# Kernel optimization log

Hardware: AMD Instinct MI355X
Metric: run time of the kernel (lower is better)

## Reference

```python
import jax, jax.numpy as jnp
import numpy as np

B, S = 128, 4096            # batch, num memory slots
W_NUM = 10000               # word_num (vocab)
CONT, FEAT, LSTM = 256, 256, 256
AH, CH = 128, 128           # actor/critic hidden dims
EPS = 1e-8


def _lin(key, out_d, in_d):
    k1, k2 = jax.random.split(key)
    s = 1.0 / np.sqrt(in_d)
    W = jax.random.uniform(k1, (out_d, in_d), jnp.float32, -s, s)
    b = jax.random.uniform(k2, (out_d,), jnp.float32, -s, s)
    return W, b


def setup_inputs() -> dict:
    key = jax.random.key(0)
    ks = jax.random.split(key, 18)
    d = {}
    d['x'] = jax.random.normal(ks[0], (B, W_NUM), jnp.float32)
    d['feat'] = jax.random.normal(ks[1], (B, S, FEAT), jnp.float32)
    d['h_tm1'] = jax.random.normal(ks[2], (B, LSTM), jnp.float32)
    d['c_tm1'] = jax.random.normal(ks[3], (B, LSTM), jnp.float32)
    d['W_x2cont'], d['b_x2cont'] = _lin(ks[4], CONT, W_NUM)
    d['W_h2cont'], d['b_h2cont'] = _lin(ks[5], CONT, LSTM)
    d['W_cont2key'], d['b_cont2key'] = _lin(ks[6], FEAT, CONT)
    d['W_cont2strength'], d['b_cont2strength'] = _lin(ks[7], 1, CONT)
    d['W_att_gates'], d['b_att_gates'] = _lin(ks[8], 1, FEAT + LSTM + CONT)
    d['W_ih'], d['b_ih'] = _lin(ks[9], 4 * LSTM, CONT + FEAT)
    d['W_hh'], d['b_hh'] = _lin(ks[10], 4 * LSTM, LSTM)
    d['W_actor_hid'], d['b_actor_hid'] = _lin(ks[11], AH, LSTM)
    d['W_critic_hid'], d['b_critic_hid'] = _lin(ks[12], CH, LSTM)
    d['W_actor'], d['b_actor'] = _lin(ks[13], W_NUM, AH)
    d['W_critic'], d['b_critic'] = _lin(ks[14], 1, CH)
    return d


def reference(x, feat, h_tm1, c_tm1,
              W_x2cont, b_x2cont, W_h2cont, b_h2cont,
              W_cont2key, b_cont2key, W_cont2strength, b_cont2strength,
              W_att_gates, b_att_gates, W_ih, b_ih, W_hh, b_hh,
              W_actor_hid, b_actor_hid, W_critic_hid, b_critic_hid,
              W_actor, b_actor, W_critic, b_critic):
    lin = lambda v, W, b: v @ W.T + b
    # controller
    x_cont = lin(x, W_x2cont, b_x2cont)                      # [B, CONT]
    h_cont = lin(h_tm1, W_h2cont, b_h2cont)                  # [B, CONT]
    control = jax.nn.relu(x_cont + h_cont)
    key_v = jnp.tanh(lin(control, W_cont2key, b_cont2key))   # [B, FEAT]
    strength = jax.nn.relu(lin(control, W_cont2strength, b_cont2strength)) + 1.0  # [B,1]
    # NTM-style content addressing: sharpened cosine similarity -> softmax over slots
    feat_n = jnp.linalg.norm(feat, axis=-1)                  # [B, S]
    key_n = jnp.linalg.norm(key_v, axis=-1, keepdims=True)   # [B, 1]
    sim = jnp.einsum('bsd,bd->bs', feat, key_v) / (feat_n * key_n + EPS)
    alpha = jax.nn.softmax(strength * sim, axis=-1)          # [B, S]
    cand_att_vec = jnp.einsum('bs,bsd->bd', alpha, feat)     # [B, FEAT]
    # attention gate
    gate_in = jnp.concatenate([cand_att_vec, h_tm1, x_cont], axis=1)  # [B, FEAT+LSTM+CONT]
    gates_att = jax.nn.sigmoid(lin(gate_in, W_att_gates, b_att_gates))
    att_vec = cand_att_vec * gates_att
    # LSTM cell (PyTorch gate order: i, f, g, o)
    inp_lstm = jnp.concatenate([att_vec, x_cont], axis=1)    # [B, FEAT+CONT]
    g = lin(inp_lstm, W_ih, b_ih) + lin(h_tm1, W_hh, b_hh)
    i, f, gg, o = jnp.split(g, 4, axis=1)
    c = jax.nn.sigmoid(f) * c_tm1 + jax.nn.sigmoid(i) * jnp.tanh(gg)
    h = jax.nn.sigmoid(o) * jnp.tanh(c)
    # heads
    action_logit = lin(jax.nn.relu(lin(h, W_actor_hid, b_actor_hid)), W_actor, b_actor)
    value = lin(jax.nn.relu(lin(h, W_critic_hid, b_critic_hid)), W_critic, b_critic)
    return (action_logit, value, h, c)
```

## Files before the change

kernel.cpp:

```cpp
#include <hip/hip_runtime.h>
#include <cmath>


#define B_ 128
#define S_ 4096
#define WN 10000
#define CD 256

__global__ __launch_bounds__(256) void k1_xcont(
    const float* __restrict__ x, const float* __restrict__ Wx,
    float* __restrict__ part) {
  const int nt = blockIdx.x;
  const int ks = blockIdx.y;
  const int t = threadIdx.x;
  __shared__ float xs[128][72];
  __shared__ float wsW[32][72];
  const int o0 = nt * 32;
  const int og = t & 7, bg = t >> 3;
  float acc[4][4] = {{0.f}};
  for (int sub = 0; sub < 4; ++sub) {
    const int k0 = ks * 256 + sub * 64;
    for (int q = t; q < 2048; q += 256) {
      const int row = q >> 4, c4 = q & 15;
      const int k = k0 + c4 * 4;
      float4 v = make_float4(0.f, 0.f, 0.f, 0.f);
      if (k < WN) v = *(const float4*)(x + (size_t)row * WN + k);
      *(float4*)&xs[row][c4 * 4] = v;
    }
    for (int q = t; q < 512; q += 256) {
      const int row = q >> 4, c4 = q & 15;
      const int k = k0 + c4 * 4;
      float4 v = make_float4(0.f, 0.f, 0.f, 0.f);
      if (k < WN) v = *(const float4*)(Wx + (size_t)(o0 + row) * WN + k);
      *(float4*)&wsW[row][c4 * 4] = v;
    }
    __syncthreads();
    for (int k = 0; k < 64; k += 4) {
      float4 wv[4];
#pragma unroll
      for (int i = 0; i < 4; ++i) wv[i] = *(const float4*)&wsW[og * 4 + i][k];
#pragma unroll
      for (int j = 0; j < 4; ++j) {
        float4 xv = *(const float4*)&xs[bg * 4 + j][k];
#pragma unroll
        for (int i = 0; i < 4; ++i)
          acc[j][i] += xv.x * wv[i].x + xv.y * wv[i].y + xv.z * wv[i].z + xv.w * wv[i].w;
      }
    }
    __syncthreads();
  }
#pragma unroll
  for (int j = 0; j < 4; ++j) {
    const int bb = bg * 4 + j;
#pragma unroll
    for (int i = 0; i < 4; ++i)
      part[(size_t)ks * 32768 + bb * 256 + o0 + og * 4 + i] = acc[j][i];
  }
}

__global__ __launch_bounds__(256) void k2_controller(
    const float* __restrict__ part, const float* __restrict__ bx,
    const float* __restrict__ h_tm1, const float* __restrict__ Wh,
    const float* __restrict__ bh, const float* __restrict__ Wk,
    const float* __restrict__ bk, const float* __restrict__ Ws,
    const float* __restrict__ bs, float* __restrict__ x_cont,
    float* __restrict__ key_v, float* __restrict__ strength,
    float* __restrict__ key_n) {
  const int b = blockIdx.x, t = threadIdx.x;
  __shared__ float hs[256], cs[256];
  __shared__ float r1[4], r2[4];
  hs[t] = h_tm1[b * 256 + t];
  float xc = bx[t];
  for (int ks = 0; ks < 40; ++ks) xc += part[(size_t)ks * 32768 + b * 256 + t];
  x_cont[b * 256 + t] = xc;
  __syncthreads();
  float hc = bh[t];
  {
    const float* w = Wh + (size_t)t * 256;
    for (int k = 0; k < 256; k += 4) {
      float4 wv = *(const float4*)(w + k);
      hc += hs[k] * wv.x + hs[k + 1] * wv.y + hs[k + 2] * wv.z + hs[k + 3] * wv.w;
    }
  }
  const float ctl = fmaxf(xc + hc, 0.f);
  cs[t] = ctl;
  __syncthreads();
  float kvv = bk[t];
  {
    const float* w = Wk + (size_t)t * 256;
    for (int k = 0; k < 256; k += 4) {
      float4 wv = *(const float4*)(w + k);
      kvv += cs[k] * wv.x + cs[k + 1] * wv.y + cs[k + 2] * wv.z + cs[k + 3] * wv.w;
    }
  }
  kvv = tanhf(kvv);
  key_v[b * 256 + t] = kvv;
  float v1 = kvv * kvv;
  float v2 = ctl * Ws[t];
  for (int off = 32; off; off >>= 1) {
    v1 += __shfl_xor(v1, off);
    v2 += __shfl_xor(v2, off);
  }
  const int w_ = t >> 6, lane = t & 63;
  if (lane == 0) { r1[w_] = v1; r2[w_] = v2; }
  __syncthreads();
  if (t == 0) {
    const float n2 = r1[0] + r1[1] + r1[2] + r1[3];
    const float sd = r2[0] + r2[1] + r2[2] + r2[3];
    key_n[b] = sqrtf(n2);
    strength[b] = fmaxf(sd + bs[0], 0.f) + 1.f;
  }
}

__global__ __launch_bounds__(256) void k3_attn(
    const float* __restrict__ feat, const float* __restrict__ key_v,
    const float* __restrict__ strength, const float* __restrict__ key_n,
    float* __restrict__ att_part) {
  const int ss = blockIdx.x;
  const int b = blockIdx.y;
  const int t = threadIdx.x;
  const int w = t >> 6, lane = t & 63;
  const float str = strength[b];
  const float kn = key_n[b];
  const float4 kv = *(const float4*)(key_v + b * 256 + lane * 4);
  const float* fb = feat + ((size_t)b * S_ + (size_t)ss * 512) * 256;
  float m = -1e30f, l = 0.f;
  float4 o = make_float4(0.f, 0.f, 0.f, 0.f);
  for (int i = 0; i < 128; ++i) {
    const float4 f = *(const float4*)(fb + (size_t)(i * 4 + w) * 256 + lane * 4);
    float d = f.x * kv.x + f.y * kv.y + f.z * kv.z + f.w * kv.w;
    float n2 = f.x * f.x + f.y * f.y + f.z * f.z + f.w * f.w;
    for (int off = 32; off; off >>= 1) {
      d += __shfl_xor(d, off);
      n2 += __shfl_xor(n2, off);
    }
    const float score = str * d / (sqrtf(n2) * kn + 1e-8f);
    const float mn = fmaxf(m, score);
    const float corr = __expf(m - mn);
    const float alpha = __expf(score - mn);
    l = l * corr + alpha;
    o.x = o.x * corr + alpha * f.x;
    o.y = o.y * corr + alpha * f.y;
    o.z = o.z * corr + alpha * f.z;
    o.w = o.w * corr + alpha * f.w;
    m = mn;
  }
  __shared__ float wm[4], wl[4];
  __shared__ float wo[4][256];
  if (lane == 0) { wm[w] = m; wl[w] = l; }
  *(float4*)&wo[w][lane * 4] = o;
  __syncthreads();
  const float mg = fmaxf(fmaxf(wm[0], wm[1]), fmaxf(wm[2], wm[3]));
  float accd = 0.f;
#pragma unroll
  for (int q = 0; q < 4; ++q) accd += wo[q][t] * __expf(wm[q] - mg);
  float* apo = att_part + (size_t)(b * 8 + ss) * 258;
  if (t == 0) {
    float lt = 0.f;
    for (int q = 0; q < 4; ++q) lt += wl[q] * __expf(wm[q] - mg);
    apo[0] = mg;
    apo[1] = lt;
  }
  apo[2 + t] = accd;
}

__global__ __launch_bounds__(256) void k4a_gate(
    const float* __restrict__ att_part, const float* __restrict__ h_tm1,
    const float* __restrict__ x_cont, const float* __restrict__ Wg,
    const float* __restrict__ bg_, float* __restrict__ inp_cat) {
  const int b = blockIdx.x, t = threadIdx.x;
  const float* ap = att_part + (size_t)b * 8 * 258;
  float mg = -1e30f;
  for (int ss = 0; ss < 8; ++ss) mg = fmaxf(mg, ap[ss * 258]);
  float lg = 0.f, od = 0.f;
  for (int ss = 0; ss < 8; ++ss) {
    const float fct = __expf(ap[ss * 258] - mg);
    lg += ap[ss * 258 + 1] * fct;
    od += ap[ss * 258 + 2 + t] * fct;
  }
  const float cand = od / lg;
  const float hv = h_tm1[b * 256 + t];
  const float xc = x_cont[b * 256 + t];
  float v = cand * Wg[t] + hv * Wg[256 + t] + xc * Wg[512 + t];
  for (int off = 32; off; off >>= 1) v += __shfl_xor(v, off);
  __shared__ float rr[4];
  __shared__ float gsh;
  const int w_ = t >> 6, lane = t & 63;
  if (lane == 0) rr[w_] = v;
  __syncthreads();
  if (t == 0) {
    const float s = rr[0] + rr[1] + rr[2] + rr[3] + bg_[0];
    gsh = 1.f / (1.f + expf(-s));
  }
  __syncthreads();
  inp_cat[b * 768 + t] = cand * gsh;
  inp_cat[b * 768 + 256 + t] = xc;
  inp_cat[b * 768 + 512 + t] = hv;
}

__global__ __launch_bounds__(256) void k4b_lstm(
    const float* __restrict__ inp_cat, const float* __restrict__ Wih,
    const float* __restrict__ bih, const float* __restrict__ Whh,
    const float* __restrict__ bhh, const float* __restrict__ c_tm1,
    float* __restrict__ h_out, float* __restrict__ c_out) {
  const int j0 = blockIdx.x * 2;
  const int t = threadIdx.x;
  __shared__ float inp_s[128][132];
  __shared__ float w_s[8][132];
  const int b = t >> 1, half = t & 1;
  float acc[4] = {0.f, 0.f, 0.f, 0.f};
  for (int kc = 0; kc < 6; ++kc) {
    const int kbase = kc * 128;
    for (int q = t; q < 4096; q += 256) {
      const int row = q >> 5, c4 = q & 31;
      *(float4*)&inp_s[row][c4 * 4] =
          *(const float4*)(inp_cat + (size_t)row * 768 + kbase + c4 * 4);
    }
    {
      const int row = t >> 5, c4 = t & 31;
      const int gate = row & 3;
      const int j = j0 + (row >> 2);
      const int og = gate * 256 + j;
      const int kg = kbase + c4 * 4;
      float4 v;
      if (kg < 512) v = *(const float4*)(Wih + (size_t)og * 512 + kg);
      else          v = *(const float4*)(Whh + (size_t)og * 256 + (kg - 512));
      *(float4*)&w_s[row][c4 * 4] = v;
    }
    __syncthreads();
    for (int k = 0; k < 128; k += 4) {
      const float4 iv = *(const float4*)&inp_s[b][k];
#pragma unroll
      for (int g = 0; g < 4; ++g) {
        const float4 wv = *(const float4*)&w_s[half * 4 + g][k];
        acc[g] += iv.x * wv.x + iv.y * wv.y + iv.z * wv.z + iv.w * wv.w;
      }
    }
    __syncthreads();
  }
  const int j = j0 + half;
  const float gi = acc[0] + bih[j] + bhh[j];
  const float gf = acc[1] + bih[256 + j] + bhh[256 + j];
  const float gg = acc[2] + bih[512 + j] + bhh[512 + j];
  const float go = acc[3] + bih[768 + j] + bhh[768 + j];
  const float ct = c_tm1[b * 256 + j];
  const float i_ = 1.f / (1.f + expf(-gi));
  const float f_ = 1.f / (1.f + expf(-gf));
  const float g_ = tanhf(gg);
  const float o_ = 1.f / (1.f + expf(-go));
  const float c = f_ * ct + i_ * g_;
  const float h = o_ * tanhf(c);
  h_out[b * 256 + j] = h;
  c_out[b * 256 + j] = c;
}

__global__ __launch_bounds__(256) void k5_hid(
    const float* __restrict__ h_in, const float* __restrict__ Wah,
    const float* __restrict__ bah, const float* __restrict__ Wch,
    const float* __restrict__ bch, float* __restrict__ hidA,
    float* __restrict__ hidC) {
  const int b = blockIdx.x, t = threadIdx.x;
  __shared__ float hs[256];
  hs[t] = h_in[b * 256 + t];
  __syncthreads();
  const float* W = (t < 128) ? (Wah + (size_t)t * 256) : (Wch + (size_t)(t - 128) * 256);
  float s = (t < 128) ? bah[t] : bch[t - 128];
  for (int k = 0; k < 256; k += 4) {
    const float4 w = *(const float4*)(W + k);
    s += hs[k] * w.x + hs[k + 1] * w.y + hs[k + 2] * w.z + hs[k + 3] * w.w;
  }
  s = fmaxf(s, 0.f);
  if (t < 128) hidA[b * 128 + t] = s;
  else         hidC[b * 128 + (t - 128)] = s;
}

__global__ __launch_bounds__(256) void k6_heads(
    const float* __restrict__ hidA, const float* __restrict__ hidC,
    const float* __restrict__ Wa, const float* __restrict__ ba,
    const float* __restrict__ Wc, const float* __restrict__ bc,
    float* __restrict__ logits, float* __restrict__ value) {
  const int t = threadIdx.x;
  if (blockIdx.x == 157) {
    if (t < 128) {
      const float* hc = hidC + (size_t)t * 128;
      float s = bc[0];
      for (int k = 0; k < 128; k += 4) {
        const float4 w = *(const float4*)(Wc + k);
        s += hc[k] * w.x + hc[k + 1] * w.y + hc[k + 2] * w.z + hc[k + 3] * w.w;
      }
      value[t] = s;
    }
    return;
  }
  const int o0 = blockIdx.x * 64;
  __shared__ float ha[128][132];
  __shared__ float wa[64][132];
  for (int q = t; q < 4096; q += 256) {
    const int row = q >> 5, c4 = q & 31;
    *(float4*)&ha[row][c4 * 4] = *(const float4*)(hidA + (size_t)row * 128 + c4 * 4);
  }
  for (int q = t; q < 2048; q += 256) {
    const int row = q >> 5, c4 = q & 31;
    const int o = o0 + row;
    float4 v = make_float4(0.f, 0.f, 0.f, 0.f);
    if (o < WN) v = *(const float4*)(Wa + (size_t)o * 128 + c4 * 4);
    *(float4*)&wa[row][c4 * 4] = v;
  }
  __syncthreads();
  const int og = t & 15, bq = t >> 4;
  float acc[8][4];
#pragma unroll
  for (int r = 0; r < 8; ++r)
#pragma unroll
    for (int i = 0; i < 4; ++i) acc[r][i] = 0.f;
  for (int k = 0; k < 128; k += 4) {
    float4 wv[4];
#pragma unroll
    for (int i = 0; i < 4; ++i) wv[i] = *(const float4*)&wa[og * 4 + i][k];
#pragma unroll
    for (int r = 0; r < 8; ++r) {
      const float4 hv = *(const float4*)&ha[bq * 8 + r][k];
#pragma unroll
      for (int i = 0; i < 4; ++i)
        acc[r][i] += hv.x * wv[i].x + hv.y * wv[i].y + hv.z * wv[i].z + hv.w * wv[i].w;
    }
  }
  const int obase = o0 + og * 4;
#pragma unroll
  for (int r = 0; r < 8; ++r) {
    const int bb = bq * 8 + r;
    if (obase + 3 < WN) {
      const float4 bias = *(const float4*)(ba + obase);
      float4 res;
      res.x = acc[r][0] + bias.x;
      res.y = acc[r][1] + bias.y;
      res.z = acc[r][2] + bias.z;
      res.w = acc[r][3] + bias.w;
      *(float4*)(logits + (size_t)bb * WN + obase) = res;
    } else {
      for (int i = 0; i < 4; ++i)
        if (obase + i < WN) logits[(size_t)bb * WN + obase + i] = acc[r][i] + ba[obase + i];
    }
  }
}

extern "C" void kernel_launch(void* const* d_in, const int* in_sizes, int n_in,
                              void* d_out, int out_size, void* d_ws, size_t ws_size,
                              hipStream_t stream) {
  const float* x     = (const float*)d_in[0];
  const float* feat  = (const float*)d_in[1];
  const float* h_tm1 = (const float*)d_in[2];
  const float* c_tm1 = (const float*)d_in[3];
  const float* Wx2c  = (const float*)d_in[4];
  const float* bx2c  = (const float*)d_in[5];
  const float* Wh2c  = (const float*)d_in[6];
  const float* bh2c  = (const float*)d_in[7];
  const float* Wc2k  = (const float*)d_in[8];
  const float* bc2k  = (const float*)d_in[9];
  const float* Wc2s  = (const float*)d_in[10];
  const float* bc2s  = (const float*)d_in[11];
  const float* Wag   = (const float*)d_in[12];
  const float* bag   = (const float*)d_in[13];
  const float* Wih   = (const float*)d_in[14];
  const float* bih   = (const float*)d_in[15];
  const float* Whh   = (const float*)d_in[16];
  const float* bhh   = (const float*)d_in[17];
  const float* Wah   = (const float*)d_in[18];
  const float* bah   = (const float*)d_in[19];
  const float* Wch   = (const float*)d_in[20];
  const float* bch   = (const float*)d_in[21];
  const float* Wa    = (const float*)d_in[22];
  const float* ba    = (const float*)d_in[23];
  const float* Wc    = (const float*)d_in[24];
  const float* bc    = (const float*)d_in[25];

  float* out    = (float*)d_out;
  float* logits = out;
  float* value  = out + 1280000;
  float* h_out  = out + 1280128;
  float* c_out  = out + 1312896;

  float* wsf      = (float*)d_ws;
  float* part     = wsf;
  float* x_cont   = part + 1310720;
  float* key_v    = x_cont + 32768;
  float* strength = key_v + 32768;
  float* key_n    = strength + 128;
  float* att_part = key_n + 128;
  float* inp_cat  = att_part + 264192;
  float* hidA     = inp_cat + 98304;
  float* hidC     = hidA + 16384;

  k1_xcont<<<dim3(8, 40), 256, 0, stream>>>(x, Wx2c, part);
  k2_controller<<<128, 256, 0, stream>>>(part, bx2c, h_tm1, Wh2c, bh2c,
                                         Wc2k, bc2k, Wc2s, bc2s,
                                         x_cont, key_v, strength, key_n);
  k3_attn<<<dim3(8, 128), 256, 0, stream>>>(feat, key_v, strength, key_n, att_part);
  k4a_gate<<<128, 256, 0, stream>>>(att_part, h_tm1, x_cont, Wag, bag, inp_cat);
  k4b_lstm<<<128, 256, 0, stream>>>(inp_cat, Wih, bih, Whh, bhh, c_tm1, h_out, c_out);
  k5_hid<<<128, 256, 0, stream>>>(h_out, Wah, bah, Wch, bch, hidA, hidC);
  k6_heads<<<158, 256, 0, stream>>>(hidA, hidC, Wa, ba, Wc, bc, logits, value);
}
```

Measured before the change: 293.3 us.

## Drop online-softmax max tracking, split attention finer, swizzle LDS in GEMMs

The attention kernel replaces online softmax with a fixed shift by the strength, which bounds the score because cosine similarity is at most one. This removes the running max and correction exponentials, and each block now covers 256 slots with two independent accumulators, launched as 16 splits. The x-projection GEMM is retiled to 16 outputs per block, giving twice as many blocks, and both it and the actor-head GEMM use XOR-swizzled float4 shared memory to avoid bank conflicts. The reduce kernel now just sums the partials. Risks include underflow if strength is large, and extra workspace for the larger partial buffer.

```diff
diff --git a/kernel.cpp b/kernel.cpp
--- a/kernel.cpp
+++ b/kernel.cpp
@@ -13,11 +13,13 @@
   const int nt = blockIdx.x;
   const int ks = blockIdx.y;
   const int t = threadIdx.x;
-  __shared__ float xs[128][72];
-  __shared__ float wsW[32][72];
-  const int o0 = nt * 32;
-  const int og = t & 7, bg = t >> 3;
-  float acc[4][4] = {{0.f}};
+  __shared__ float4 xs[128][16];
+  __shared__ float4 wsW[16][16];
+  const int o0 = nt * 16;
+  const int og = t & 3;
+  const int bg = t >> 2;
+  const int bgx = bg & 7;
+  float acc[2][4] = {{0.f, 0.f, 0.f, 0.f}, {0.f, 0.f, 0.f, 0.f}};
   for (int sub = 0; sub < 4; ++sub) {
     const int k0 = ks * 256 + sub * 64;
     for (int q = t; q < 2048; q += 256) {
@@ -25,23 +27,24 @@
       const int k = k0 + c4 * 4;
       float4 v = make_float4(0.f, 0.f, 0.f, 0.f);
       if (k < WN) v = *(const float4*)(x + (size_t)row * WN + k);
-      *(float4*)&xs[row][c4 * 4] = v;
-    }
-    for (int q = t; q < 512; q += 256) {
-      const int row = q >> 4, c4 = q & 15;
+      xs[row][c4 ^ (row & 7)] = v;
+    }
+    {
+      const int row = t >> 4, c4 = t & 15;
       const int k = k0 + c4 * 4;
       float4 v = make_float4(0.f, 0.f, 0.f, 0.f);
       if (k < WN) v = *(const float4*)(Wx + (size_t)(o0 + row) * WN + k);
-      *(float4*)&wsW[row][c4 * 4] = v;
+      wsW[row][c4 ^ (row & 7)] = v;
     }
     __syncthreads();
-    for (int k = 0; k < 64; k += 4) {
+#pragma unroll
+    for (int c4 = 0; c4 < 16; ++c4) {
       float4 wv[4];
 #pragma unroll
-      for (int i = 0; i < 4; ++i) wv[i] = *(const float4*)&wsW[og * 4 + i][k];
-#pragma unroll
-      for (int j = 0; j < 4; ++j) {
-        float4 xv = *(const float4*)&xs[bg * 4 + j][k];
+      for (int i = 0; i < 4; ++i) wv[i] = wsW[og * 4 + i][c4 ^ ((og * 4 + i) & 7)];
+#pragma unroll
+      for (int j = 0; j < 2; ++j) {
+        const float4 xv = xs[bg + j * 64][c4 ^ bgx];
 #pragma unroll
         for (int i = 0; i < 4; ++i)
           acc[j][i] += xv.x * wv[i].x + xv.y * wv[i].y + xv.z * wv[i].z + xv.w * wv[i].w;
@@ -50,8 +53,8 @@
     __syncthreads();
   }
 #pragma unroll
-  for (int j = 0; j < 4; ++j) {
-    const int bb = bg * 4 + j;
+  for (int j = 0; j < 2; ++j) {
+    const int bb = bg + j * 64;
 #pragma unroll
     for (int i = 0; i < 4; ++i)
       part[(size_t)ks * 32768 + bb * 256 + o0 + og * 4 + i] = acc[j][i];
@@ -112,7 +115,7 @@
   }
 }
 
-__global__ __launch_bounds__(256) void k3_attn(
+__global__ __launch_bounds__(256, 8) void k3_attn(
     const float* __restrict__ feat, const float* __restrict__ key_v,
     const float* __restrict__ strength, const float* __restrict__ key_n,
     float* __restrict__ att_part) {
@@ -123,45 +126,41 @@
   const float str = strength[b];
   const float kn = key_n[b];
   const float4 kv = *(const float4*)(key_v + b * 256 + lane * 4);
-  const float* fb = feat + ((size_t)b * S_ + (size_t)ss * 512) * 256;
-  float m = -1e30f, l = 0.f;
-  float4 o = make_float4(0.f, 0.f, 0.f, 0.f);
-  for (int i = 0; i < 128; ++i) {
-    const float4 f = *(const float4*)(fb + (size_t)(i * 4 + w) * 256 + lane * 4);
-    float d = f.x * kv.x + f.y * kv.y + f.z * kv.z + f.w * kv.w;
-    float n2 = f.x * f.x + f.y * f.y + f.z * f.z + f.w * f.w;
+  const float* fb = feat + ((size_t)b * S_ + (size_t)ss * 256) * 256;
+  float l0 = 0.f, l1 = 0.f;
+  float4 o0 = make_float4(0.f, 0.f, 0.f, 0.f);
+  float4 o1 = make_float4(0.f, 0.f, 0.f, 0.f);
+  for (int i = 0; i < 32; ++i) {
+    const float4 fA = *(const float4*)(fb + (size_t)((i * 2) * 4 + w) * 256 + lane * 4);
+    const float4 fB = *(const float4*)(fb + (size_t)((i * 2 + 1) * 4 + w) * 256 + lane * 4);
+    float dA = fA.x * kv.x + fA.y * kv.y + fA.z * kv.z + fA.w * kv.w;
+    float nA = fA.x * fA.x + fA.y * fA.y + fA.z * fA.z + fA.w * fA.w;
+    float dB = fB.x * kv.x + fB.y * kv.y + fB.z * kv.z + fB.w * kv.w;
+    float nB = fB.x * fB.x + fB.y * fB.y + fB.z * fB.z + fB.w * fB.w;
+#pragma unroll
     for (int off = 32; off; off >>= 1) {
-      d += __shfl_xor(d, off);
-      n2 += __shfl_xor(n2, off);
-    }
-    const float score = str * d / (sqrtf(n2) * kn + 1e-8f);
-    const float mn = fmaxf(m, score);
-    const float corr = __expf(m - mn);
-    const float alpha = __expf(score - mn);
-    l = l * corr + alpha;
-    o.x = o.x * corr + alpha * f.x;
-    o.y = o.y * corr + alpha * f.y;
-    o.z = o.z * corr + alpha * f.z;
-    o.w = o.w * corr + alpha * f.w;
-    m = mn;
-  }
-  __shared__ float wm[4], wl[4];
+      dA += __shfl_xor(dA, off); nA += __shfl_xor(nA, off);
+      dB += __shfl_xor(dB, off); nB += __shfl_xor(nB, off);
+    }
+    const float sA = str * dA / (sqrtf(nA) * kn + 1e-8f);
+    const float sB = str * dB / (sqrtf(nB) * kn + 1e-8f);
+    const float aA = __expf(sA - str);
+    const float aB = __expf(sB - str);
+    l0 += aA; l1 += aB;
+    o0.x += aA * fA.x; o0.y += aA * fA.y; o0.z += aA * fA.z; o0.w += aA * fA.w;
+    o1.x += aB * fB.x; o1.y += aB * fB.y; o1.z += aB * fB.z; o1.w += aB * fB.w;
+  }
+  __shared__ float wl[4];
   __shared__ float wo[4][256];
-  if (lane == 0) { wm[w] = m; wl[w] = l; }
-  *(float4*)&wo[w][lane * 4] = o;
-  __syncthreads();
-  const float mg = fmaxf(fmaxf(wm[0], wm[1]), fmaxf(wm[2], wm[3]));
-  float accd = 0.f;
-#pragma unroll
-  for (int q = 0; q < 4; ++q) accd += wo[q][t] * __expf(wm[q] - mg);
-  float* apo = att_part + (size_t)(b * 8 + ss) * 258;
-  if (t == 0) {
-    float lt = 0.f;
-    for (int q = 0; q < 4; ++q) lt += wl[q] * __expf(wm[q] - mg);
-    apo[0] = mg;
-    apo[1] = lt;
-  }
-  apo[2 + t] = accd;
+  if (lane == 0) wl[w] = l0 + l1;
+  float4 os;
+  os.x = o0.x + o1.x; os.y = o0.y + o1.y; os.z = o0.z + o1.z; os.w = o0.w + o1.w;
+  *(float4*)&wo[w][lane * 4] = os;
+  __syncthreads();
+  const float od = wo[0][t] + wo[1][t] + wo[2][t] + wo[3][t];
+  float* apo = att_part + (size_t)(b * 16 + ss) * 264;
+  if (t == 0) apo[0] = wl[0] + wl[1] + wl[2] + wl[3];
+  apo[4 + t] = od;
 }
 
 __global__ __launch_bounds__(256) void k4a_gate(
@@ -169,14 +168,12 @@
     const float* __restrict__ x_cont, const float* __restrict__ Wg,
     const float* __restrict__ bg_, float* __restrict__ inp_cat) {
   const int b = blockIdx.x, t = threadIdx.x;
-  const float* ap = att_part + (size_t)b * 8 * 258;
-  float mg = -1e30f;
-  for (int ss = 0; ss < 8; ++ss) mg = fmaxf(mg, ap[ss * 258]);
+  const float* ap = att_part + (size_t)b * 16 * 264;
   float lg = 0.f, od = 0.f;
-  for (int ss = 0; ss < 8; ++ss) {
-    const float fct = __expf(ap[ss * 258] - mg);
-    lg += ap[ss * 258 + 1] * fct;
-    od += ap[ss * 258 + 2 + t] * fct;
+#pragma unroll
+  for (int ss = 0; ss < 16; ++ss) {
+    lg += ap[ss * 264];
+    od += ap[ss * 264 + 4 + t];
   }
   const float cand = od / lg;
   const float hv = h_tm1[b * 256 + t];
@@ -293,18 +290,18 @@
     return;
   }
   const int o0 = blockIdx.x * 64;
-  __shared__ float ha[128][132];
-  __shared__ float wa[64][132];
+  __shared__ float4 ha[128][32];
+  __shared__ float4 wa[64][32];
   for (int q = t; q < 4096; q += 256) {
     const int row = q >> 5, c4 = q & 31;
-    *(float4*)&ha[row][c4 * 4] = *(const float4*)(hidA + (size_t)row * 128 + c4 * 4);
+    ha[row][c4 ^ ((row >> 2) & 7)] = *(const float4*)(hidA + (size_t)row * 128 + c4 * 4);
   }
   for (int q = t; q < 2048; q += 256) {
     const int row = q >> 5, c4 = q & 31;
     const int o = o0 + row;
     float4 v = make_float4(0.f, 0.f, 0.f, 0.f);
     if (o < WN) v = *(const float4*)(Wa + (size_t)o * 128 + c4 * 4);
-    *(float4*)&wa[row][c4 * 4] = v;
+    wa[row][c4 ^ ((row >> 2) & 7)] = v;
   }
   __syncthreads();
   const int og = t & 15, bq = t >> 4;
@@ -313,13 +310,14 @@
   for (int r = 0; r < 8; ++r)
 #pragma unroll
     for (int i = 0; i < 4; ++i) acc[r][i] = 0.f;
-  for (int k = 0; k < 128; k += 4) {
+#pragma unroll 4
+  for (int c4 = 0; c4 < 32; ++c4) {
     float4 wv[4];
 #pragma unroll
-    for (int i = 0; i < 4; ++i) wv[i] = *(const float4*)&wa[og * 4 + i][k];
+    for (int i = 0; i < 4; ++i) wv[i] = wa[og * 4 + i][c4 ^ (og & 7)];
 #pragma unroll
     for (int r = 0; r < 8; ++r) {
-      const float4 hv = *(const float4*)&ha[bq * 8 + r][k];
+      const float4 hv = ha[bq * 8 + r][c4 ^ ((bq * 2 + (r >> 2)) & 7)];
 #pragma unroll
       for (int i = 0; i < 4; ++i)
         acc[r][i] += hv.x * wv[i].x + hv.y * wv[i].y + hv.z * wv[i].z + hv.w * wv[i].w;
@@ -387,15 +385,15 @@
   float* strength = key_v + 32768;
   float* key_n    = strength + 128;
   float* att_part = key_n + 128;
-  float* inp_cat  = att_part + 264192;
+  float* inp_cat  = att_part + 540672;
   float* hidA     = inp_cat + 98304;
   float* hidC     = hidA + 16384;
 
-  k1_xcont<<<dim3(8, 40), 256, 0, stream>>>(x, Wx2c, part);
+  k1_xcont<<<dim3(16, 40), 256, 0, stream>>>(x, Wx2c, part);
   k2_controller<<<128, 256, 0, stream>>>(part, bx2c, h_tm1, Wh2c, bh2c,
                                          Wc2k, bc2k, Wc2s, bc2s,
                                          x_cont, key_v, strength, key_n);
-  k3_attn<<<dim3(8, 128), 256, 0, stream>>>(feat, key_v, strength, key_n, att_part);
+  k3_attn<<<dim3(16, 128), 256, 0, stream>>>(feat, key_v, strength, key_n, att_part);
   k4a_gate<<<128, 256, 0, stream>>>(att_part, h_tm1, x_cont, Wag, bag, inp_cat);
   k4b_lstm<<<128, 256, 0, stream>>>(inp_cat, Wih, bih, Whh, bhh, c_tm1, h_out, c_out);
   k5_hid<<<128, 256, 0, stream>>>(h_out, Wah, bah, Wch, bch, hidA, hidC);
```

New measurement: 285.7 us. 1.03x faster.
